# Kernel optimization log

Hardware: AMD Instinct MI355X
Metric: run time of the kernel (lower is better)

Reference implementation:

```python
import jax, jax.numpy as jnp
import numpy as np
from jax import lax

N, D, H, O = 16384, 512, 1024, 512
G, E, K = 3, 4, 2
ALPHA = 0.01


def setup_inputs() -> dict:
    key = jax.random.key(0)
    ks = jax.random.split(key, 16)

    def lin(k, out_d, in_d):
        s = 1.0 / np.sqrt(in_d)
        return jax.random.uniform(k, (out_d, in_d), jnp.float32, -s, s)

    x = jax.random.normal(ks[0], (N, D), jnp.float32)
    Wm = lin(ks[1], G, D)
    bm = jnp.zeros((G,), jnp.float32)
    # group routers stacked: [G, E, D]
    Wr = jax.random.uniform(ks[2], (G, E, D), jnp.float32, -1 / np.sqrt(D), 1 / np.sqrt(D))
    br = jnp.zeros((G, E), jnp.float32)
    # expert params stacked over (group, expert)
    W1 = jax.random.uniform(ks[3], (G, E, H, D), jnp.float32, -1 / np.sqrt(D), 1 / np.sqrt(D))
    b1 = jnp.zeros((G, E, H), jnp.float32)
    W2 = jax.random.uniform(ks[4], (G, E, H, H), jnp.float32, -1 / np.sqrt(H), 1 / np.sqrt(H))
    b2 = jnp.zeros((G, E, H), jnp.float32)
    Wp = jax.random.uniform(ks[5], (G, E, H, D), jnp.float32, -1 / np.sqrt(D), 1 / np.sqrt(D))
    bp = jnp.zeros((G, E, H), jnp.float32)
    W3 = jax.random.uniform(ks[6], (G, E, O, H), jnp.float32, -1 / np.sqrt(H), 1 / np.sqrt(H))
    b3 = jnp.zeros((G, E, O), jnp.float32)
    return {"x": x, "Wm": Wm, "bm": bm, "Wr": Wr, "br": br,
            "W1": W1, "b1": b1, "W2": W2, "b2": b2,
            "Wp": Wp, "bp": bp, "W3": W3, "b3": b3}


def _expert(x, W1, b1, W2, b2, Wp, bp, W3, b3):
    # residual MLP (dropout in eval mode => identity)
    h = jax.nn.relu(x @ W1.T + b1)
    h = h @ W2.T + b2
    ident = x @ Wp.T + bp  # projection (input_dim != hidden_dim)
    h = jax.nn.relu(h + ident)
    return h @ W3.T + b3


def reference(x, Wm, bm, Wr, br, W1, b1, W2, b2, Wp, bp, W3, b3):
    n = x.shape[0]
    # ---- meta (top-1 group) routing ----
    meta_logits = x @ Wm.T + bm                         # [N, G]
    g = jnp.argmax(meta_logits, axis=1)                 # top-1 group per token
    pm = jax.nn.softmax(meta_logits, axis=1).mean(0)    # [G]
    aux = ALPHA * G * jnp.sum(pm * pm)
    # ---- per-group router logits, gathered for each token's group ----
    logits_all = jnp.einsum('nd,ged->nge', x, Wr) + br  # [N, G, E]
    sel = jnp.take_along_axis(logits_all, g[:, None, None], axis=1)[:, 0, :]  # [N, E]
    # ---- group-level load-balancing aux loss (over tokens in each group) ----
    probs = jax.nn.softmax(sel, axis=-1)                # [N, E]
    onehot_g = (g[:, None] == jnp.arange(G)[None, :])   # [N, G] bool
    cnt = onehot_g.sum(0)                               # [G]
    mean_g = (onehot_g.astype(x.dtype).T @ probs) / jnp.maximum(cnt, 1)[:, None].astype(x.dtype)
    aux = aux + jnp.sum(jnp.where(cnt > 0, ALPHA * E * jnp.sum(mean_g * mean_g, -1), 0.0))
    # ---- top-k expert weights within selected group (softmax over the k logits) ----
    vals, idx = lax.top_k(sel, K)                       # [N, K]
    w = jax.nn.softmax(vals, axis=-1)                   # [N, K]
    cw = jnp.zeros((n, E), x.dtype).at[jnp.arange(n)[:, None], idx].set(w)   # [N, E]
    combine = cw[:, None, :] * onehot_g[:, :, None].astype(x.dtype)          # [N, G, E]
    # ---- expert compute + combine (loop over the fixed small set of experts) ----
    out = jnp.zeros((n, O), x.dtype)
    for gi in range(G):
        for e in range(E):
            y = _expert(x, W1[gi, e], b1[gi, e], W2[gi, e], b2[gi, e],
                        Wp[gi, e], bp[gi, e], W3[gi, e], b3[gi, e])
            out = out + combine[:, gi, e:e + 1] * y
    return out, aux
```

## Files before the change

kernel.cpp:

```cpp
#include <hip/hip_runtime.h>
#include <hip/hip_bf16.h>

#define N_TOK 16384
#define DDIM  512
#define HDIM  1024
#define ODIM  512
#define NG    3
#define NE    4
#define NGE   12
#define TASK_CAP 272

typedef __bf16 bf16x8 __attribute__((ext_vector_type(8)));
typedef float  f32x4  __attribute__((ext_vector_type(4)));
typedef unsigned int u32;

__device__ __forceinline__ void gld_lds16(const void* gsrc, void* ldst) {
    __builtin_amdgcn_global_load_lds(
        (const __attribute__((address_space(1))) u32*)gsrc,
        (__attribute__((address_space(3))) u32*)ldst, 16, 0, 0);
}

static constexpr size_t OFF_WSLOT = 512;
static constexpr size_t OFF_ELIST = OFF_WSLOT + (size_t)N_TOK*2*4;
static constexpr size_t OFF_TASK  = 917504;
static constexpr size_t OFF_XBF   = 1048576;
static constexpr size_t OFF_W1    = OFF_XBF + (size_t)N_TOK*DDIM*2;
static constexpr size_t OFF_W2    = OFF_W1  + (size_t)NGE*HDIM*DDIM*2;
static constexpr size_t OFF_WP    = OFF_W2  + (size_t)NGE*HDIM*HDIM*2;
static constexpr size_t OFF_W3    = OFF_WP  + (size_t)NGE*HDIM*DDIM*2;
static constexpr size_t OFF_H1    = OFF_W3  + (size_t)NGE*ODIM*HDIM*2;
static constexpr size_t OFF_U     = OFF_H1  + (size_t)N_TOK*2*HDIM*2;
static constexpr size_t OFF_Y     = OFF_U   + (size_t)N_TOK*2*HDIM*2;
static constexpr size_t WS_NEED   = OFF_Y   + (size_t)N_TOK*2*ODIM*2;

__global__ void cast_all_k(const float* __restrict__ x,  const float* __restrict__ w1,
                           const float* __restrict__ w2, const float* __restrict__ wp,
                           const float* __restrict__ w3,
                           __bf16* xbf, __bf16* w1b, __bf16* w2b, __bf16* wpb, __bf16* w3b) {
    int tid = blockIdx.x * blockDim.x + threadIdx.x;
    int stride = gridDim.x * blockDim.x;
    auto seg = [&](const float* __restrict__ s, __bf16* __restrict__ d, int n4) {
        const float4* s4 = (const float4*)s;
        uint2* d4 = (uint2*)d;
        for (int i = tid; i < n4; i += stride) {
            float4 v = s4[i];
            union { __bf16 h[4]; uint2 u; } o;
            o.h[0] = (__bf16)v.x; o.h[1] = (__bf16)v.y;
            o.h[2] = (__bf16)v.z; o.h[3] = (__bf16)v.w;
            d4[i] = o.u;
        }
    };
    seg(x,  xbf, N_TOK*DDIM/4);
    seg(w1, w1b, NGE*HDIM*DDIM/4);
    seg(w2, w2b, NGE*HDIM*HDIM/4);
    seg(wp, wpb, NGE*HDIM*DDIM/4);
    seg(w3, w3b, NGE*ODIM*HDIM/4);
}

__global__ __launch_bounds__(256) void routing_k(
        const float* __restrict__ x,  const float* __restrict__ Wm,
        const float* __restrict__ bm, const float* __restrict__ Wr,
        const float* __restrict__ br,
        float* pmsum, float* psum, int* cnt, int* ecount,
        int* elist, float* wslot) {
    __shared__ float lpm[NG];
    __shared__ float lpsum[NGE];
    __shared__ int   lcnt[NG];
    __shared__ int   lec[NGE];
    __shared__ int   lbase[NGE];
    __shared__ int   lentry[NGE][64];

    int tid = threadIdx.x;
    if (tid < NG)  { lpm[tid] = 0.f; lcnt[tid] = 0; }
    if (tid < NGE) { lpsum[tid] = 0.f; lec[tid] = 0; }
    __syncthreads();

    int wid = tid >> 6, lane = tid & 63;

    #pragma unroll 1
    for (int i = 0; i < 16; ++i) {
        int t = blockIdx.x * 64 + i * 4 + wid;

        const float4* xr = (const float4*)(x + (size_t)t * DDIM);
        float4 xa = xr[lane*2], xb = xr[lane*2+1];

        float meta[NG];
        #pragma unroll
        for (int gi = 0; gi < NG; ++gi) {
            const float4* w = (const float4*)(Wm + gi*DDIM);
            float4 wa = w[lane*2], wb = w[lane*2+1];
            float s = xa.x*wa.x + xa.y*wa.y + xa.z*wa.z + xa.w*wa.w
                    + xb.x*wb.x + xb.y*wb.y + xb.z*wb.z + xb.w*wb.w;
            #pragma unroll
            for (int off = 32; off > 0; off >>= 1) s += __shfl_xor(s, off);
            meta[gi] = s + bm[gi];
        }
        int g = 0;
        if (meta[1] > meta[g]) g = 1;
        if (meta[2] > meta[g]) g = 2;

        float mm = fmaxf(meta[0], fmaxf(meta[1], meta[2]));
        float e0 = expf(meta[0]-mm), e1 = expf(meta[1]-mm), e2 = expf(meta[2]-mm);
        float inv = 1.f / (e0 + e1 + e2);

        float sel[NE];
        #pragma unroll
        for (int e = 0; e < NE; ++e) {
            const float4* w = (const float4*)(Wr + (size_t)(g*NE + e)*DDIM);
            float4 wa = w[lane*2], wb = w[lane*2+1];
            float s = xa.x*wa.x + xa.y*wa.y + xa.z*wa.z + xa.w*wa.w
                    + xb.x*wb.x + xb.y*wb.y + xb.z*wb.z + xb.w*wb.w;
            #pragma unroll
            for (int off = 32; off > 0; off >>= 1) s += __shfl_xor(s, off);
            sel[e] = s + br[g*NE + e];
        }
        float ms = fmaxf(fmaxf(sel[0],sel[1]), fmaxf(sel[2],sel[3]));
        float pe[NE]; float ss = 0.f;
        #pragma unroll
        for (int e = 0; e < NE; ++e) { pe[e] = expf(sel[e]-ms); ss += pe[e]; }
        float invs = 1.f / ss;

        int i0 = 0;
        #pragma unroll
        for (int e = 1; e < NE; ++e) if (sel[e] > sel[i0]) i0 = e;
        int i1 = (i0 == 0) ? 1 : 0;
        #pragma unroll
        for (int e = 0; e < NE; ++e) if (e != i0 && sel[e] > sel[i1]) i1 = e;
        float ew = expf(sel[i1] - sel[i0]);
        float wden = 1.f / (1.f + ew);

        if (lane == 0) {
            atomicAdd(&lpm[0], e0*inv);
            atomicAdd(&lpm[1], e1*inv);
            atomicAdd(&lpm[2], e2*inv);
            #pragma unroll
            for (int e = 0; e < NE; ++e) atomicAdd(&lpsum[g*NE + e], pe[e]*invs);
            atomicAdd(&lcnt[g], 1);
            int ee0 = g*NE + i0, ee1 = g*NE + i1;
            int p0 = atomicAdd(&lec[ee0], 1);
            lentry[ee0][p0] = t*2;
            int p1 = atomicAdd(&lec[ee1], 1);
            lentry[ee1][p1] = t*2 + 1;
            wslot[t*2]   = wden;
            wslot[t*2+1] = ew * wden;
        }
    }
    __syncthreads();

    if (tid < NG)  { atomicAdd(pmsum + tid, lpm[tid]); atomicAdd(cnt + tid, lcnt[tid]); }
    if (tid < NGE) { atomicAdd(psum + tid, lpsum[tid]);
                     lbase[tid] = atomicAdd(ecount + tid, lec[tid]); }
    __syncthreads();

    for (int e = wid; e < NGE; e += 4) {
        int c = lec[e], base = lbase[e];
        for (int j = lane; j < c; j += 64)
            elist[e*N_TOK + base + j] = lentry[e][j];
    }
}

__global__ void finalize_aux_k(const float* pmsum, const float* psum, const int* cnt,
                               const int* ecount, int2* tasks, int* ntasks,
                               float* outAux) {
    if (threadIdx.x != 0 || blockIdx.x != 0) return;
    float s = 0.f;
    for (int i = 0; i < NG; ++i) { float p = pmsum[i] / (float)N_TOK; s += p*p; }
    float aux = 0.01f * NG * s;
    for (int gg = 0; gg < NG; ++gg) {
        int c = cnt[gg];
        if (c > 0) {
            float s2 = 0.f;
            for (int e = 0; e < NE; ++e) { float m = psum[gg*NE+e] / (float)c; s2 += m*m; }
            aux += 0.01f * NE * s2;
        }
    }
    *outAux = aux;
    int nt = 0;
    for (int ge = 0; ge < NGE; ++ge) {
        int c = ecount[ge];
        for (int m0 = 0; m0 < c; m0 += 128) tasks[nt++] = make_int2(ge, m0);
    }
    *ntasks = nt;
}

template<int NDIM, bool RELU, bool TWOPASS>
__global__ __launch_bounds__(256) void expert_gemm_k(
        const __bf16* __restrict__ A1, int shift1, int k1, const __bf16* __restrict__ B1,
        const __bf16* __restrict__ A2, int shift2, int k2, const __bf16* __restrict__ B2,
        const float* __restrict__ bias1, const float* __restrict__ bias2,
        __bf16* __restrict__ Out,
        const int* __restrict__ ecount, const int* __restrict__ elist,
        const int2* __restrict__ tasks, const int* __restrict__ ntasks) {
    constexpr int NPAN = NDIM / 128;
    constexpr int PSH  = (NPAN == 8) ? 3 : 2;
    int T = *ntasks;
    int q = T >> 3, r = T & 7;
    int xcd  = blockIdx.x & 7;
    int idx  = blockIdx.x >> 3;
    int tloc = idx >> PSH;
    int panel = idx & (NPAN - 1);
    int cx = q + (xcd < r ? 1 : 0);
    if (tloc >= cx) return;
    int task = (xcd < r ? xcd * (q + 1) : r * (q + 1) + (xcd - r) * q) + tloc;
    int2 tk = tasks[task];
    int ge = tk.x, m0 = tk.y;
    int cntE = ecount[ge];
    int n0 = panel * 128;

    __shared__ __align__(16) char ldsA[3][8192];
    __shared__ __align__(16) char ldsB[3][8192];
    __shared__ int ents[128];

    int tid = threadIdx.x;
    if (tid < 128) {
        int rr = m0 + tid;
        if (rr >= cntE) rr = cntE - 1;
        ents[tid] = elist[ge*N_TOK + rr];
    }
    __syncthreads();

    int lane = tid & 63, wv = tid >> 6;
    int wm = wv >> 1, wn = wv & 1;
    int lr = lane & 15, lg = lane >> 4;
    int cr = lane >> 2;
    int csw = (lane & 3) ^ ((lane >> 3) & 3);

    const char* sA1[2]; const char* sB1[2];
    const char* sA2[2]; const char* sB2[2];
    size_t rowB1 = (size_t)k1 * 2;
    #pragma unroll
    for (int j = 0; j < 2; ++j) {
        sA1[j] = (const char*)A1 + (size_t)(ents[32*wv + 16*j + cr] >> shift1) * rowB1 + csw*16;
        sB1[j] = (const char*)(B1 + (size_t)(ge*NDIM + n0 + 32*wv + 16*j + cr) * k1) + csw*16;
    }
    int nk1 = k1 >> 5;
    int H = nk1;
    if constexpr (TWOPASS) {
        size_t rowB2 = (size_t)k2 * 2;
        #pragma unroll
        for (int j = 0; j < 2; ++j) {
            sA2[j] = (const char*)A2 + (size_t)(ents[32*wv + 16*j + cr] >> shift2) * rowB2 + csw*16;
            sB2[j] = (const char*)(B2 + (size_t)(ge*NDIM + n0 + 32*wv + 16*j + cr) * k2) + csw*16;
        }
        H += (k2 >> 5);
    }

    auto stage = [&](int h) {
        int qb = h % 3;
        char* dA = ldsA[qb] + wv*2048;
        char* dB = ldsB[qb] + wv*2048;
        if (!TWOPASS || h < nk1) {
            size_t off = (size_t)h << 6;
            gld_lds16(sA1[0] + off, dA);
            gld_lds16(sA1[1] + off, dA + 1024);
            gld_lds16(sB1[0] + off, dB);
            gld_lds16(sB1[1] + off, dB + 1024);
        } else {
            size_t off = (size_t)(h - nk1) << 6;
            gld_lds16(sA2[0] + off, dA);
            gld_lds16(sA2[1] + off, dA + 1024);
            gld_lds16(sB2[0] + off, dB);
            gld_lds16(sB2[1] + off, dB + 1024);
        }
    };

    f32x4 acc[4][4] = {};

    stage(0);
    stage(1);
    asm volatile("s_waitcnt vmcnt(4)" ::: "memory");
    __builtin_amdgcn_s_barrier();

    #pragma unroll 1
    for (int s = 0; s < H; ++s) {
        if (s + 2 < H) stage(s + 2);

        const char* bA = ldsA[s % 3];
        const char* bB = ldsB[s % 3];
        bf16x8 av[4], bv[4];
        #pragma unroll
        for (int mi = 0; mi < 4; ++mi) {
            int ar = wm*64 + mi*16 + lr;
            av[mi] = *(const bf16x8*)(bA + ar*64 + ((lg ^ ((ar >> 1) & 3)) << 4));
        }
        #pragma unroll
        for (int ni = 0; ni < 4; ++ni) {
            int br_ = wn*64 + ni*16 + lr;
            bv[ni] = *(const bf16x8*)(bB + br_*64 + ((lg ^ ((br_ >> 1) & 3)) << 4));
        }
        #pragma unroll
        for (int mi = 0; mi < 4; ++mi)
            #pragma unroll
            for (int ni = 0; ni < 4; ++ni)
                acc[mi][ni] = __builtin_amdgcn_mfma_f32_16x16x32_bf16(
                    av[mi], bv[ni], acc[mi][ni], 0, 0, 0);

        if (s + 2 < H)      asm volatile("s_waitcnt vmcnt(4)" ::: "memory");
        else                asm volatile("s_waitcnt vmcnt(0)" ::: "memory");
        __builtin_amdgcn_s_barrier();
    }

    #pragma unroll
    for (int ni = 0; ni < 4; ++ni) {
        int col = n0 + wn*64 + ni*16 + lr;
        float b = bias1[(size_t)ge*NDIM + col];
        if constexpr (TWOPASS) b += bias2[(size_t)ge*NDIM + col];
        #pragma unroll
        for (int mi = 0; mi < 4; ++mi) {
            #pragma unroll
            for (int j = 0; j < 4; ++j) {
                int rloc = wm*64 + mi*16 + lg*4 + j;
                if (m0 + rloc < cntE) {
                    float v = acc[mi][ni][j] + b;
                    if constexpr (RELU) v = fmaxf(v, 0.f);
                    Out[(size_t)ents[rloc] * NDIM + col] = (__bf16)v;
                }
            }
        }
    }
}

__global__ void combine_k(const __bf16* __restrict__ Y, const float* __restrict__ wslot,
                          float* __restrict__ out) {
    int idx = blockIdx.x * blockDim.x + threadIdx.x;
    int t = idx >> 6;
    int o = (idx & 63) * 8;
    bf16x8 y0 = *(const bf16x8*)(Y + (size_t)(2*t)   * ODIM + o);
    bf16x8 y1 = *(const bf16x8*)(Y + (size_t)(2*t+1) * ODIM + o);
    float w0 = wslot[2*t], w1 = wslot[2*t+1];
    float4 r0, r1;
    r0.x = w0*(float)y0[0] + w1*(float)y1[0];
    r0.y = w0*(float)y0[1] + w1*(float)y1[1];
    r0.z = w0*(float)y0[2] + w1*(float)y1[2];
    r0.w = w0*(float)y0[3] + w1*(float)y1[3];
    r1.x = w0*(float)y0[4] + w1*(float)y1[4];
    r1.y = w0*(float)y0[5] + w1*(float)y1[5];
    r1.z = w0*(float)y0[6] + w1*(float)y1[6];
    r1.w = w0*(float)y0[7] + w1*(float)y1[7];
    float* op = out + (size_t)t * ODIM + o;
    ((float4*)op)[0] = r0;
    ((float4*)op)[1] = r1;
}

extern "C" void kernel_launch(void* const* d_in, const int* in_sizes, int n_in,
                              void* d_out, int out_size, void* d_ws, size_t ws_size,
                              hipStream_t stream) {
    const float* x  = (const float*)d_in[0];
    const float* Wm = (const float*)d_in[1];
    const float* bm = (const float*)d_in[2];
    const float* Wr = (const float*)d_in[3];
    const float* br = (const float*)d_in[4];
    const float* W1 = (const float*)d_in[5];
    const float* b1 = (const float*)d_in[6];
    const float* W2 = (const float*)d_in[7];
    const float* b2 = (const float*)d_in[8];
    const float* Wp = (const float*)d_in[9];
    const float* bp = (const float*)d_in[10];
    const float* W3 = (const float*)d_in[11];
    const float* b3 = (const float*)d_in[12];

    if (ws_size < WS_NEED) return;

    char* ws = (char*)d_ws;
    float* outp = (float*)d_out;

    float* pmsum  = (float*)ws;
    float* psum   = (float*)ws + 4;
    int*   cnt    = (int*)ws + 16;
    int*   ecount = (int*)ws + 20;
    int*   ntasks = (int*)ws + 34;
    float* wslot  = (float*)(ws + OFF_WSLOT);
    int*   elist  = (int*)(ws + OFF_ELIST);
    int2*  tasks  = (int2*)(ws + OFF_TASK);
    __bf16* xbf = (__bf16*)(ws + OFF_XBF);
    __bf16* w1b = (__bf16*)(ws + OFF_W1);
    __bf16* w2b = (__bf16*)(ws + OFF_W2);
    __bf16* wpb = (__bf16*)(ws + OFF_WP);
    __bf16* w3b = (__bf16*)(ws + OFF_W3);
    __bf16* H1  = (__bf16*)(ws + OFF_H1);
    __bf16* U   = (__bf16*)(ws + OFF_U);
    __bf16* Y   = (__bf16*)(ws + OFF_Y);

    hipMemsetAsync(d_ws, 0, 512, stream);

    cast_all_k<<<4096, 256, 0, stream>>>(x, W1, W2, Wp, W3, xbf, w1b, w2b, wpb, w3b);

    routing_k<<<256, 256, 0, stream>>>(x, Wm, bm, Wr, br,
                                       pmsum, psum, cnt, ecount, elist, wslot);

    finalize_aux_k<<<1, 64, 0, stream>>>(pmsum, psum, cnt, ecount, tasks, ntasks,
                                         outp + (size_t)N_TOK*ODIM);

    expert_gemm_k<HDIM, true, false><<<TASK_CAP*(HDIM/128), 256, 0, stream>>>(
        xbf, 1, DDIM, w1b, nullptr, 0, 0, nullptr, b1, nullptr, H1,
        ecount, elist, tasks, ntasks);

    expert_gemm_k<HDIM, true, true><<<TASK_CAP*(HDIM/128), 256, 0, stream>>>(
        H1, 0, HDIM, w2b, xbf, 1, DDIM, wpb, b2, bp, U,
        ecount, elist, tasks, ntasks);

    expert_gemm_k<ODIM, false, false><<<TASK_CAP*(ODIM/128), 256, 0, stream>>>(
        U, 0, HDIM, w3b, nullptr, 0, 0, nullptr, b3, nullptr, Y,
        ecount, elist, tasks, ntasks);

    combine_k<<<4096, 256, 0, stream>>>(Y, wslot, outp);
}
```

Measured before the change: 403.1 us.

## Merge cast into routing kernel and fuse combine into final GEMM via atomics

The bf16 cast kernel and the routing kernel become one launch, with extra blocks past index 256 doing the casts while the first 256 blocks do routing. The separate combine kernel and the Y intermediate buffer are removed. The last expert GEMM now scales each result by its routing weight and atomically adds it into a zeroed fp32 output, which adds a memset of the output. This cuts launches and a round trip of Y through memory, but relies on fp32 atomics with 2-way contention and scattered per-element writes, and summation order is no longer deterministic.

```diff
diff --git a/kernel.cpp b/kernel.cpp
--- a/kernel.cpp
+++ b/kernel.cpp
@@ -30,37 +30,15 @@
 static constexpr size_t OFF_W3    = OFF_WP  + (size_t)NGE*HDIM*DDIM*2;
 static constexpr size_t OFF_H1    = OFF_W3  + (size_t)NGE*ODIM*HDIM*2;
 static constexpr size_t OFF_U     = OFF_H1  + (size_t)N_TOK*2*HDIM*2;
-static constexpr size_t OFF_Y     = OFF_U   + (size_t)N_TOK*2*HDIM*2;
-static constexpr size_t WS_NEED   = OFF_Y   + (size_t)N_TOK*2*ODIM*2;
-
-__global__ void cast_all_k(const float* __restrict__ x,  const float* __restrict__ w1,
-                           const float* __restrict__ w2, const float* __restrict__ wp,
-                           const float* __restrict__ w3,
-                           __bf16* xbf, __bf16* w1b, __bf16* w2b, __bf16* wpb, __bf16* w3b) {
-    int tid = blockIdx.x * blockDim.x + threadIdx.x;
-    int stride = gridDim.x * blockDim.x;
-    auto seg = [&](const float* __restrict__ s, __bf16* __restrict__ d, int n4) {
-        const float4* s4 = (const float4*)s;
-        uint2* d4 = (uint2*)d;
-        for (int i = tid; i < n4; i += stride) {
-            float4 v = s4[i];
-            union { __bf16 h[4]; uint2 u; } o;
-            o.h[0] = (__bf16)v.x; o.h[1] = (__bf16)v.y;
-            o.h[2] = (__bf16)v.z; o.h[3] = (__bf16)v.w;
-            d4[i] = o.u;
-        }
-    };
-    seg(x,  xbf, N_TOK*DDIM/4);
-    seg(w1, w1b, NGE*HDIM*DDIM/4);
-    seg(w2, w2b, NGE*HDIM*HDIM/4);
-    seg(wp, wpb, NGE*HDIM*DDIM/4);
-    seg(w3, w3b, NGE*ODIM*HDIM/4);
-}
-
-__global__ __launch_bounds__(256) void routing_k(
+static constexpr size_t WS_NEED   = OFF_U   + (size_t)N_TOK*2*HDIM*2;
+
+__global__ __launch_bounds__(256) void prep_k(
         const float* __restrict__ x,  const float* __restrict__ Wm,
         const float* __restrict__ bm, const float* __restrict__ Wr,
         const float* __restrict__ br,
+        const float* __restrict__ w1, const float* __restrict__ w2,
+        const float* __restrict__ wp, const float* __restrict__ w3,
+        __bf16* xbf, __bf16* w1b, __bf16* w2b, __bf16* wpb, __bf16* w3b,
         float* pmsum, float* psum, int* cnt, int* ecount,
         int* elist, float* wslot) {
     __shared__ float lpm[NG];
@@ -71,6 +49,30 @@
     __shared__ int   lentry[NGE][64];
 
     int tid = threadIdx.x;
+
+    if (blockIdx.x >= 256) {
+        int cbid = blockIdx.x - 256;
+        int ctid = cbid * 256 + tid;
+        int stride = (gridDim.x - 256) * 256;
+        auto seg = [&](const float* __restrict__ s, __bf16* __restrict__ d, int n4) {
+            const float4* s4 = (const float4*)s;
+            uint2* d4 = (uint2*)d;
+            for (int i = ctid; i < n4; i += stride) {
+                float4 v = s4[i];
+                union { __bf16 h[4]; uint2 u; } o;
+                o.h[0] = (__bf16)v.x; o.h[1] = (__bf16)v.y;
+                o.h[2] = (__bf16)v.z; o.h[3] = (__bf16)v.w;
+                d4[i] = o.u;
+            }
+        };
+        seg(x,  xbf, N_TOK*DDIM/4);
+        seg(w1, w1b, NGE*HDIM*DDIM/4);
+        seg(w2, w2b, NGE*HDIM*HDIM/4);
+        seg(wp, wpb, NGE*HDIM*DDIM/4);
+        seg(w3, w3b, NGE*ODIM*HDIM/4);
+        return;
+    }
+
     if (tid < NG)  { lpm[tid] = 0.f; lcnt[tid] = 0; }
     if (tid < NGE) { lpsum[tid] = 0.f; lec[tid] = 0; }
     __syncthreads();
@@ -183,12 +185,13 @@
     *ntasks = nt;
 }
 
-template<int NDIM, bool RELU, bool TWOPASS>
+template<int NDIM, bool RELU, bool TWOPASS, bool COMBINE>
 __global__ __launch_bounds__(256) void expert_gemm_k(
         const __bf16* __restrict__ A1, int shift1, int k1, const __bf16* __restrict__ B1,
         const __bf16* __restrict__ A2, int shift2, int k2, const __bf16* __restrict__ B2,
         const float* __restrict__ bias1, const float* __restrict__ bias2,
-        __bf16* __restrict__ Out,
+        __bf16* __restrict__ Out, const float* __restrict__ wslot,
+        float* __restrict__ outp,
         const int* __restrict__ ecount, const int* __restrict__ elist,
         const int2* __restrict__ tasks, const int* __restrict__ ntasks) {
     constexpr int NPAN = NDIM / 128;
@@ -210,12 +213,15 @@
     __shared__ __align__(16) char ldsA[3][8192];
     __shared__ __align__(16) char ldsB[3][8192];
     __shared__ int ents[128];
+    __shared__ float wsl[128];
 
     int tid = threadIdx.x;
     if (tid < 128) {
         int rr = m0 + tid;
         if (rr >= cntE) rr = cntE - 1;
-        ents[tid] = elist[ge*N_TOK + rr];
+        int e = elist[ge*N_TOK + rr];
+        ents[tid] = e;
+        if constexpr (COMBINE) wsl[tid] = wslot[e];
     }
     __syncthreads();
 
@@ -313,33 +319,16 @@
                 if (m0 + rloc < cntE) {
                     float v = acc[mi][ni][j] + b;
                     if constexpr (RELU) v = fmaxf(v, 0.f);
-                    Out[(size_t)ents[rloc] * NDIM + col] = (__bf16)v;
+                    if constexpr (COMBINE) {
+                        int ent = ents[rloc];
+                        atomicAdd(outp + (size_t)(ent >> 1) * ODIM + col, wsl[rloc] * v);
+                    } else {
+                        Out[(size_t)ents[rloc] * NDIM + col] = (__bf16)v;
+                    }
                 }
             }
         }
     }
-}
-
-__global__ void combine_k(const __bf16* __restrict__ Y, const float* __restrict__ wslot,
-                          float* __restrict__ out) {
-    int idx = blockIdx.x * blockDim.x + threadIdx.x;
-    int t = idx >> 6;
-    int o = (idx & 63) * 8;
-    bf16x8 y0 = *(const bf16x8*)(Y + (size_t)(2*t)   * ODIM + o);
-    bf16x8 y1 = *(const bf16x8*)(Y + (size_t)(2*t+1) * ODIM + o);
-    float w0 = wslot[2*t], w1 = wslot[2*t+1];
-    float4 r0, r1;
-    r0.x = w0*(float)y0[0] + w1*(float)y1[0];
-    r0.y = w0*(float)y0[1] + w1*(float)y1[1];
-    r0.z = w0*(float)y0[2] + w1*(float)y1[2];
-    r0.w = w0*(float)y0[3] + w1*(float)y1[3];
-    r1.x = w0*(float)y0[4] + w1*(float)y1[4];
-    r1.y = w0*(float)y0[5] + w1*(float)y1[5];
-    r1.z = w0*(float)y0[6] + w1*(float)y1[6];
-    r1.w = w0*(float)y0[7] + w1*(float)y1[7];
-    float* op = out + (size_t)t * ODIM + o;
-    ((float4*)op)[0] = r0;
-    ((float4*)op)[1] = r1;
 }
 
 extern "C" void kernel_launch(void* const* d_in, const int* in_sizes, int n_in,
@@ -379,29 +368,26 @@
     __bf16* w3b = (__bf16*)(ws + OFF_W3);
     __bf16* H1  = (__bf16*)(ws + OFF_H1);
     __bf16* U   = (__bf16*)(ws + OFF_U);
-    __bf16* Y   = (__bf16*)(ws + OFF_Y);
 
     hipMemsetAsync(d_ws, 0, 512, stream);
-
-    cast_all_k<<<4096, 256, 0, stream>>>(x, W1, W2, Wp, W3, xbf, w1b, w2b, wpb, w3b);
-
-    routing_k<<<256, 256, 0, stream>>>(x, Wm, bm, Wr, br,
-                                       pmsum, psum, cnt, ecount, elist, wslot);
+    hipMemsetAsync(d_out, 0, (size_t)N_TOK * ODIM * 4, stream);
+
+    prep_k<<<4352, 256, 0, stream>>>(x, Wm, bm, Wr, br, W1, W2, Wp, W3,
+                                     xbf, w1b, w2b, wpb, w3b,
+                                     pmsum, psum, cnt, ecount, elist, wslot);
 
     finalize_aux_k<<<1, 64, 0, stream>>>(pmsum, psum, cnt, ecount, tasks, ntasks,
                                          outp + (size_t)N_TOK*ODIM);
 
-    expert_gemm_k<HDIM, true, false><<<TASK_CAP*(HDIM/128), 256, 0, stream>>>(
-        xbf, 1, DDIM, w1b, nullptr, 0, 0, nullptr, b1, nullptr, H1,
+    expert_gemm_k<HDIM, true, false, false><<<TASK_CAP*(HDIM/128), 256, 0, stream>>>(
+        xbf, 1, DDIM, w1b, nullptr, 0, 0, nullptr, b1, nullptr, H1, nullptr, nullptr,
         ecount, elist, tasks, ntasks);
 
-    expert_gemm_k<HDIM, true, true><<<TASK_CAP*(HDIM/128), 256, 0, stream>>>(
-        H1, 0, HDIM, w2b, xbf, 1, DDIM, wpb, b2, bp, U,
+    expert_gemm_k<HDIM, true, true, false><<<TASK_CAP*(HDIM/128), 256, 0, stream>>>(
+        H1, 0, HDIM, w2b, xbf, 1, DDIM, wpb, b2, bp, U, nullptr, nullptr,
         ecount, elist, tasks, ntasks);
 
-    expert_gemm_k<ODIM, false, false><<<TASK_CAP*(ODIM/128), 256, 0, stream>>>(
-        U, 0, HDIM, w3b, nullptr, 0, 0, nullptr, b3, nullptr, Y,
+    expert_gemm_k<ODIM, false, false, true><<<TASK_CAP*(ODIM/128), 256, 0, stream>>>(
+        U, 0, HDIM, w3b, nullptr, 0, 0, nullptr, b3, nullptr, nullptr, wslot, outp,
         ecount, elist, tasks, ntasks);
-
-    combine_k<<<4096, 256, 0, stream>>>(Y, wslot, outp);
-}
+}
```

After: 435.2 us. 8.0% more time.
